# Performance work log

Measured on AMD Instinct MI355X. Metric: run time of the kernel, lower is better.

## Reference

```python
import jax, jax.numpy as jnp
import numpy as np

B, T, D = 1, 2048, 2048
H, HD = 16, 128          # n_heads, head_dim
RD = 64                  # rotary_emb_dim
K = 4                    # short conv kernel size
EPS = 1e-5


def setup_inputs() -> dict:
    key = jax.random.key(0)
    ks = jax.random.split(key, 10)
    hidden_states = jax.random.normal(ks[0], (B, T, D), dtype=jnp.float32)
    # standard RoPE tables for the rotary sub-dimension
    inv_freq = 1.0 / (10000.0 ** (jnp.arange(0, RD, 2, dtype=jnp.float32) / RD))  # [RD/2]
    pos = jnp.arange(T, dtype=jnp.float32)
    freqs = pos[:, None] * inv_freq[None, :]          # [T, RD/2]
    emb = jnp.concatenate([freqs, freqs], axis=-1)    # [T, RD]
    cos = jnp.broadcast_to(jnp.cos(emb)[None], (B, T, RD))
    sin = jnp.broadcast_to(jnp.sin(emb)[None], (B, T, RD))
    s = 1.0 / np.sqrt(D)
    return {
        "hidden_states": hidden_states,
        "cos": cos, "sin": sin,
        "Wq": jax.random.normal(ks[1], (D, D), jnp.float32) * s,
        "Wk": jax.random.normal(ks[2], (D, D), jnp.float32) * s,
        "Wv": jax.random.normal(ks[3], (D, D), jnp.float32) * s,
        "Wo": jax.random.normal(ks[4], (D, D), jnp.float32) * s,
        "conv_q_w": jax.random.normal(ks[5], (D, K), jnp.float32) * 0.5,
        "conv_k_w": jax.random.normal(ks[6], (D, K), jnp.float32) * 0.5,
        "conv_v_w": jax.random.normal(ks[7], (D, K), jnp.float32) * 0.5,
        "q_norm_w": jnp.ones((HD,), jnp.float32),
        "k_norm_w": jnp.ones((HD,), jnp.float32),
    }


def _causal_conv_silu(x, w):
    # x: [B,T,D], w: [D,K]; depthwise causal conv (tap K-1 hits current pos) + SiLU
    xp = jnp.pad(x, ((0, 0), (K - 1, 0), (0, 0)))
    y = sum(xp[:, j:j + T, :] * w[None, None, :, j] for j in range(K))
    return jax.nn.silu(y)


def _rms_norm(x, w):
    # x: [..., HD]
    var = jnp.mean(x * x, axis=-1, keepdims=True)
    return x * jax.lax.rsqrt(var + EPS) * w


def _rotate_half(x):
    x1, x2 = x[..., : x.shape[-1] // 2], x[..., x.shape[-1] // 2:]
    return jnp.concatenate([-x2, x1], axis=-1)


def _apply_rope(x, cos, sin):
    # x: [B,H,T,HD]; cos/sin: [B,T,RD] -> unsqueeze head dim; partial rotary branch
    cos = cos[:, None, :, :]
    sin = sin[:, None, :, :]
    x_rot, x_pass = x[..., :RD], x[..., RD:]
    x_rot = x_rot * cos + _rotate_half(x_rot) * sin
    # faithful to source: negates rotated part when rotary_dim != head_dim
    return jnp.concatenate([-x_rot, x_pass], axis=-1)


def reference(hidden_states, cos, sin, Wq, Wk, Wv, Wo,
              conv_q_w, conv_k_w, conv_v_w, q_norm_w, k_norm_w):
    # projections (Linear with bias=False: y = x @ W^T)
    q = hidden_states @ Wq.T
    k = hidden_states @ Wk.T
    v = hidden_states @ Wv.T
    # short causal depthwise conv + SiLU
    q = _causal_conv_silu(q, conv_q_w)
    k = _causal_conv_silu(k, conv_k_w)
    v = _causal_conv_silu(v, conv_v_w)
    # split heads: [B,T,D] -> [B,T,H,HD]
    q = q.reshape(B, T, H, HD)
    k = k.reshape(B, T, H, HD)
    v = v.reshape(B, T, H, HD)
    # per-head RMSNorm, then [B,H,T,HD]
    q = _rms_norm(q, q_norm_w).transpose(0, 2, 1, 3)
    k = _rms_norm(k, k_norm_w).transpose(0, 2, 1, 3)
    v = v.transpose(0, 2, 1, 3)
    # RoPE (partial)
    q = _apply_rope(q, cos, sin)
    k = _apply_rope(k, cos, sin)
    # causal attention
    scale = 1.0 / np.sqrt(HD)
    scores = jnp.einsum('bhqd,bhkd->bhqk', q, k) * scale
    causal = jnp.tril(jnp.ones((T, T), dtype=bool))
    scores = jnp.where(causal[None, None], scores, jnp.float32(-1e30))
    probs = jax.nn.softmax(scores, axis=-1)
    attn = jnp.einsum('bhqk,bhkd->bhqd', probs, v)
    # [B,H,T,HD] -> [B,T,D], output projection
    out = attn.transpose(0, 2, 1, 3).reshape(B, T, D) @ Wo.T
    return out
```

## Files before the change

kernel.cpp:

```cpp
#include <hip/hip_runtime.h>
#include <hip/hip_bf16.h>

#define T_SEQ 2048
#define D_MODEL 2048
#define NH 16
#define HDIM 128
#define RD_ROT 64

typedef __bf16 bf16x8 __attribute__((ext_vector_type(8)));
typedef float f32x4 __attribute__((ext_vector_type(4)));

__device__ __forceinline__ void async_copy16(const __bf16* g, __bf16* l) {
    __builtin_amdgcn_global_load_lds(
        (const __attribute__((address_space(1))) void*)g,
        (__attribute__((address_space(3))) void*)l, 16, 0, 0);
}

__global__ __launch_bounds__(256) void cast_kernel(
    const float* __restrict__ s0, const float* __restrict__ s1, const float* __restrict__ s2,
    const float* __restrict__ s3, const float* __restrict__ s4,
    __bf16* __restrict__ d0, __bf16* __restrict__ d1, __bf16* __restrict__ d2,
    __bf16* __restrict__ d3, __bf16* __restrict__ d4)
{
    const float* s; __bf16* d;
    switch (blockIdx.y) {
        case 0: s = s0; d = d0; break;
        case 1: s = s1; d = d1; break;
        case 2: s = s2; d = d2; break;
        case 3: s = s3; d = d3; break;
        default: s = s4; d = d4; break;
    }
    size_t base = (size_t)blockIdx.x * D_MODEL + (size_t)threadIdx.x * 8;
    f32x4 a = *(const f32x4*)(s + base);
    f32x4 b = *(const f32x4*)(s + base + 4);
    bf16x8 o;
    #pragma unroll
    for (int i = 0; i < 4; i++) { o[i] = (__bf16)a[i]; o[i + 4] = (__bf16)b[i]; }
    *(bf16x8*)(d + base) = o;
}

__device__ __forceinline__ bf16x8 ld_frag(const __bf16* lds, int rr, int s, int quad, int r7) {
    return *(const bf16x8*)&lds[rr * 64 + ((((s << 2) + quad) ^ r7) << 3)];
}

__global__ __launch_bounds__(512, 2) void gemm_qkv_8ph_kernel(
    const __bf16* __restrict__ A,
    const __bf16* __restrict__ B0, const __bf16* __restrict__ B1, const __bf16* __restrict__ B2,
    __bf16* __restrict__ C0, __bf16* __restrict__ C1, __bf16* __restrict__ C2)
{
    constexpr int BM = 256, BK = 64, KD = D_MODEL, NT = KD / BK;

    __shared__ __align__(16) __bf16 As[2][BM * BK];
    __shared__ __align__(16) __bf16 Bs[2][BM * BK];

    const int flat = (int)blockIdx.x + 8 * ((int)blockIdx.y + 8 * (int)blockIdx.z);
    const int swz  = (flat & 7) * 24 + (flat >> 3);
    const int bz   = swz >> 6;
    const int bm   = (swz & 7) * BM;
    const int bn   = ((swz >> 3) & 7) * BM;

    const __bf16* Bmat = bz == 0 ? B0 : (bz == 1 ? B1 : B2);
    __bf16* Cmat       = bz == 0 ? C0 : (bz == 1 ? C1 : C2);

    const int tid  = threadIdx.x;
    const int lane = tid & 63;
    const int wave = tid >> 6;
    const int r15  = lane & 15;
    const int quad = lane >> 4;
    const int r7   = r15 & 7;
    const int wm   = wave >> 2;
    const int wn   = wave & 3;

    const int sr8 = lane >> 3;
    const int sck = (lane & 7) ^ sr8;
    const __bf16* Ap = A    + (size_t)(bm + wave * 16 + sr8) * KD + sck * 8;
    const __bf16* Bp = Bmat + (size_t)(bn + wave * 16 + sr8) * KD + sck * 8;

    auto stageA = [&](int buf, int h, int kt) {
        const __bf16* s = Ap + (size_t)(h * 128) * KD + kt;
        __bf16* d = &As[buf][h * 8192 + wave * 1024];
        async_copy16(s, d);
        async_copy16(s + 8 * KD, d + 512);
    };
    auto stageB = [&](int buf, int h, int kt) {
        const __bf16* s = Bp + (size_t)(h * 128) * KD + kt;
        __bf16* d = &Bs[buf][h * 8192 + wave * 1024];
        async_copy16(s, d);
        async_copy16(s + 8 * KD, d + 512);
    };

    f32x4 acc[8][4] = {};

    stageA(0, 0, 0);  stageA(0, 1, 0);  stageB(0, 0, 0);  stageB(0, 1, 0);
    stageA(1, 0, BK); stageA(1, 1, BK); stageB(1, 0, BK); stageB(1, 1, BK);
    asm volatile("s_waitcnt vmcnt(8)" ::: "memory");
    __builtin_amdgcn_s_barrier();

    for (int t = 0; t < NT; t++) {
        const int b = t & 1;
        const __bf16* Asb = As[b];
        const __bf16* Bsb = Bs[b];
        const bool pf = (t + 2 < NT);
        const int ktp = (t + 2) * BK;

        bf16x8 a0[4][2], a1[4][2], b0[2][2], b1[2][2];

        #pragma unroll
        for (int mf = 0; mf < 4; mf++)
            #pragma unroll
            for (int s = 0; s < 2; s++)
                a0[mf][s] = ld_frag(Asb, wm * 128 + mf * 16 + r15, s, quad, r7);
        #pragma unroll
        for (int nf = 0; nf < 2; nf++)
            #pragma unroll
            for (int s = 0; s < 2; s++)
                b0[nf][s] = ld_frag(Bsb, wn * 64 + nf * 16 + r15, s, quad, r7);
        __builtin_amdgcn_s_barrier();
        asm volatile("s_waitcnt lgkmcnt(0)" ::: "memory");
        __builtin_amdgcn_sched_barrier(0);
        __builtin_amdgcn_s_setprio(1);
        #pragma unroll
        for (int mf = 0; mf < 4; mf++)
            #pragma unroll
            for (int nf = 0; nf < 2; nf++)
                #pragma unroll
                for (int s = 0; s < 2; s++)
                    acc[mf][nf] = __builtin_amdgcn_mfma_f32_16x16x32_bf16(a0[mf][s], b0[nf][s], acc[mf][nf], 0, 0, 0);
        __builtin_amdgcn_s_setprio(0);
        __builtin_amdgcn_sched_barrier(0);
        __builtin_amdgcn_s_barrier();

        #pragma unroll
        for (int mf = 0; mf < 4; mf++)
            #pragma unroll
            for (int s = 0; s < 2; s++)
                a1[mf][s] = ld_frag(Asb, wm * 128 + 64 + mf * 16 + r15, s, quad, r7);
        #pragma unroll
        for (int nf = 0; nf < 2; nf++)
            #pragma unroll
            for (int s = 0; s < 2; s++)
                b1[nf][s] = ld_frag(Bsb, wn * 64 + 32 + nf * 16 + r15, s, quad, r7);
        __builtin_amdgcn_s_barrier();
        asm volatile("s_waitcnt lgkmcnt(0)" ::: "memory");
        __builtin_amdgcn_sched_barrier(0);
        __builtin_amdgcn_s_setprio(1);
        #pragma unroll
        for (int mf = 0; mf < 4; mf++)
            #pragma unroll
            for (int nf = 0; nf < 2; nf++)
                #pragma unroll
                for (int s = 0; s < 2; s++)
                    acc[4 + mf][2 + nf] = __builtin_amdgcn_mfma_f32_16x16x32_bf16(a1[mf][s], b1[nf][s], acc[4 + mf][2 + nf], 0, 0, 0);
        __builtin_amdgcn_s_setprio(0);
        __builtin_amdgcn_sched_barrier(0);
        __builtin_amdgcn_s_barrier();

        if (pf) { stageA(b, 0, ktp); stageB(b, 0, ktp); }
        __builtin_amdgcn_s_barrier();
        __builtin_amdgcn_s_setprio(1);
        #pragma unroll
        for (int mf = 0; mf < 4; mf++)
            #pragma unroll
            for (int nf = 0; nf < 2; nf++)
                #pragma unroll
                for (int s = 0; s < 2; s++)
                    acc[mf][2 + nf] = __builtin_amdgcn_mfma_f32_16x16x32_bf16(a0[mf][s], b1[nf][s], acc[mf][2 + nf], 0, 0, 0);
        __builtin_amdgcn_s_setprio(0);
        __builtin_amdgcn_sched_barrier(0);
        __builtin_amdgcn_s_barrier();

        if (pf) { stageA(b, 1, ktp); stageB(b, 1, ktp); }
        __builtin_amdgcn_s_barrier();
        __builtin_amdgcn_s_setprio(1);
        #pragma unroll
        for (int mf = 0; mf < 4; mf++)
            #pragma unroll
            for (int nf = 0; nf < 2; nf++)
                #pragma unroll
                for (int s = 0; s < 2; s++)
                    acc[4 + mf][nf] = __builtin_amdgcn_mfma_f32_16x16x32_bf16(a1[mf][s], b0[nf][s], acc[4 + mf][nf], 0, 0, 0);
        __builtin_amdgcn_s_setprio(0);
        __builtin_amdgcn_sched_barrier(0);
        if (t + 1 < NT) {
            if (pf) asm volatile("s_waitcnt vmcnt(8)" ::: "memory");
            else    asm volatile("s_waitcnt vmcnt(0)" ::: "memory");
        }
        __builtin_amdgcn_s_barrier();
    }

    #pragma unroll
    for (int mf = 0; mf < 8; mf++) {
        #pragma unroll
        for (int r = 0; r < 4; r++) {
            const size_t row = (size_t)(bm + wm * 128 + mf * 16 + quad * 4 + r);
            #pragma unroll
            for (int nf = 0; nf < 4; nf++) {
                const size_t col = (size_t)(bn + wn * 64 + nf * 16 + r15);
                Cmat[row * D_MODEL + col] = (__bf16)acc[mf][nf][r];
            }
        }
    }
}

__global__ __launch_bounds__(256) void gemm_bt_splitk_kernel(
    const __bf16* __restrict__ A, const __bf16* __restrict__ Bm, float* __restrict__ C)
{
    constexpr int BM = 128, BK = 32, KD = D_MODEL, NIT = (KD / 2) / BK;
    __shared__ __align__(16) __bf16 As[2][BM * BK];
    __shared__ __align__(16) __bf16 Bs[2][BM * BK];

    const int lane = threadIdx.x & 63;
    const int wave = threadIdx.x >> 6;
    const int r15  = lane & 15;
    const int quad = lane >> 4;
    const int bm = blockIdx.x * BM;
    const int bn = blockIdx.y * BM;
    const int wm = (wave >> 1) * 64;
    const int wn = (wave & 1) * 64;
    const int kbase = blockIdx.z * (KD / 2);

    f32x4 acc[4][4] = {};
    const int srow = wave * 32 + (lane >> 2);
    const int sg   = (lane & 3) ^ ((lane >> 2) & 3);

    const __bf16* Arow0 = A  + (size_t)(bm + srow)      * KD + kbase + sg * 8;
    const __bf16* Arow1 = A  + (size_t)(bm + srow + 16) * KD + kbase + sg * 8;
    const __bf16* Brow0 = Bm + (size_t)(bn + srow)      * KD + kbase + sg * 8;
    const __bf16* Brow1 = Bm + (size_t)(bn + srow + 16) * KD + kbase + sg * 8;

    async_copy16(Arow0, &As[0][wave * 1024]);
    async_copy16(Arow1, &As[0][wave * 1024 + 512]);
    async_copy16(Brow0, &Bs[0][wave * 1024]);
    async_copy16(Brow1, &Bs[0][wave * 1024 + 512]);

    for (int it = 0; it < NIT; it++) {
        const int buf = it & 1;
        __syncthreads();

        if (it + 1 < NIT) {
            const int k0 = (it + 1) * BK;
            const int nb = buf ^ 1;
            async_copy16(Arow0 + k0, &As[nb][wave * 1024]);
            async_copy16(Arow1 + k0, &As[nb][wave * 1024 + 512]);
            async_copy16(Brow0 + k0, &Bs[nb][wave * 1024]);
            async_copy16(Brow1 + k0, &Bs[nb][wave * 1024 + 512]);
        }

        bf16x8 av[4], bv[4];
        #pragma unroll
        for (int mt = 0; mt < 4; mt++)
            av[mt] = *(const bf16x8*)&As[buf][(wm + mt * 16 + r15) * BK + ((quad ^ (r15 & 3)) << 3)];
        #pragma unroll
        for (int nt = 0; nt < 4; nt++)
            bv[nt] = *(const bf16x8*)&Bs[buf][(wn + nt * 16 + r15) * BK + ((quad ^ (r15 & 3)) << 3)];
        #pragma unroll
        for (int mt = 0; mt < 4; mt++)
            #pragma unroll
            for (int nt = 0; nt < 4; nt++)
                acc[mt][nt] = __builtin_amdgcn_mfma_f32_16x16x32_bf16(av[mt], bv[nt], acc[mt][nt], 0, 0, 0);
    }

    #pragma unroll
    for (int mt = 0; mt < 4; mt++) {
        #pragma unroll
        for (int r = 0; r < 4; r++) {
            size_t row = bm + wm + mt * 16 + quad * 4 + r;
            #pragma unroll
            for (int nt = 0; nt < 4; nt++) {
                size_t col = bn + wn + nt * 16 + r15;
                atomicAdd(&C[row * D_MODEL + col], acc[mt][nt][r]);
            }
        }
    }
}

__global__ __launch_bounds__(256) void preproc_qk_kernel(
    const __bf16* __restrict__ q_raw, const __bf16* __restrict__ k_raw,
    const float* __restrict__ cwq, const float* __restrict__ cwk,
    const float* __restrict__ qnw, const float* __restrict__ knw,
    const float* __restrict__ cosb, const float* __restrict__ sinb,
    __bf16* __restrict__ q_proc, __bf16* __restrict__ k_proc)
{
    const int t = blockIdx.x;
    const int which = blockIdx.y;
    const __bf16* X = which ? k_raw : q_raw;
    const float*  W = which ? cwk : cwq;
    const float*  nw = which ? knw : qnw;
    __bf16* P = which ? k_proc : q_proc;
    const float SC = which ? 1.0f : 0.08838834764831845f;

    const int tid = threadIdx.x;
    const int c0  = tid * 8;
    const int h   = tid >> 4;
    const int dl0 = (tid & 15) * 8;

    f32x4 wv[8];
    #pragma unroll
    for (int i = 0; i < 8; i++) wv[i] = *(const f32x4*)&W[(c0 + i) * 4];

    float acc[8] = {};
    #pragma unroll
    for (int j = 0; j < 4; j++) {
        int tt = t + j - 3;
        if (tt >= 0) {
            bf16x8 xv = *(const bf16x8*)&X[(size_t)tt * D_MODEL + c0];
            #pragma unroll
            for (int i = 0; i < 8; i++) acc[i] += (float)xv[i] * wv[i][j];
        }
    }
    float sil[8], ss = 0.f;
    #pragma unroll
    for (int i = 0; i < 8; i++) {
        float s = acc[i] / (1.f + __expf(-acc[i]));
        sil[i] = s; ss += s * s;
    }
    #pragma unroll
    for (int off = 1; off < 16; off <<= 1) ss += __shfl_xor(ss, off);
    float inv = rsqrtf(ss * (1.f / 128.f) + 1e-5f);

    f32x4 nv0 = *(const f32x4*)&nw[dl0];
    f32x4 nv1 = *(const f32x4*)&nw[dl0 + 4];
    float yn[8];
    #pragma unroll
    for (int i = 0; i < 8; i++) yn[i] = sil[i] * inv * (i < 4 ? nv0[i] : nv1[i - 4]);

    float partner[8];
    #pragma unroll
    for (int i = 0; i < 8; i++) partner[i] = __shfl_xor(yn[i], 4);

    bf16x8 o;
    if (dl0 < RD_ROT) {
        f32x4 cv0 = *(const f32x4*)&cosb[t * RD_ROT + dl0];
        f32x4 cv1 = *(const f32x4*)&cosb[t * RD_ROT + dl0 + 4];
        f32x4 sv0 = *(const f32x4*)&sinb[t * RD_ROT + dl0];
        f32x4 sv1 = *(const f32x4*)&sinb[t * RD_ROT + dl0 + 4];
        #pragma unroll
        for (int i = 0; i < 8; i++) {
            int dl = dl0 + i;
            float c = i < 4 ? cv0[i] : cv1[i - 4];
            float s = i < 4 ? sv0[i] : sv1[i - 4];
            float rot = (dl < 32) ? -partner[i] : partner[i];
            o[i] = (__bf16)((yn[i] * c + rot * s) * SC);
        }
    } else {
        #pragma unroll
        for (int i = 0; i < 8; i++) o[i] = (__bf16)(yn[i] * SC);
    }
    *(bf16x8*)&P[((size_t)h * T_SEQ + t) * HDIM + dl0] = o;
}

__global__ __launch_bounds__(128) void preproc_v_kernel(
    const __bf16* __restrict__ v_raw, const float* __restrict__ cwv,
    __bf16* __restrict__ v_t)
{
    const int t0 = blockIdx.x * 8;
    const int h = blockIdx.y;
    const int dl = threadIdx.x;
    const int d = h * HDIM + dl;

    f32x4 wv = *(const f32x4*)&cwv[d * 4];
    float x[11];
    #pragma unroll
    for (int m = 0; m < 11; m++) {
        int tt = t0 - 3 + m;
        x[m] = (tt >= 0) ? (float)v_raw[(size_t)tt * D_MODEL + d] : 0.f;
    }
    bf16x8 o;
    #pragma unroll
    for (int r = 0; r < 8; r++) {
        float y = x[r] * wv[0] + x[r + 1] * wv[1] + x[r + 2] * wv[2] + x[r + 3] * wv[3];
        o[r] = (__bf16)(y / (1.f + __expf(-y)));
    }
    *(bf16x8*)&v_t[((size_t)h * HDIM + dl) * T_SEQ + t0] = o;
}

__global__ __launch_bounds__(256, 2) void attn_kernel(
    const __bf16* __restrict__ Qp,
    const __bf16* __restrict__ Kp,
    const __bf16* __restrict__ Vt,
    __bf16* __restrict__ Op)
{
    constexpr int TK = 64, PSTR = 72;
    __shared__ __align__(16) __bf16 Ks[2][TK * HDIM];
    __shared__ __align__(16) __bf16 Vs[2][HDIM * TK];
    __shared__ __align__(16) __bf16 Ps[64 * PSTR];

    const int lane = threadIdx.x & 63;
    const int wave = threadIdx.x >> 6;
    const int r15  = lane & 15;
    const int quad = lane >> 4;
    const int h = blockIdx.y;
    const int qi = (blockIdx.y & 8) ? ((int)gridDim.x - 1 - (int)blockIdx.x) : (int)blockIdx.x;
    const int q0 = qi * TK;

    const __bf16* Kb = Kp + (size_t)h * T_SEQ * HDIM;
    const __bf16* Vb = Vt + (size_t)h * HDIM * T_SEQ;

    const int kchunk = wave * 4;
    const int krow_l = (lane >> 4);
    const int kg     = lane & 15;
    const int vrow_l = (lane >> 3);
    const int vg     = lane & 7;

    bf16x8 qf[4];
    const __bf16* qbase = Qp + ((size_t)h * T_SEQ + q0 + wave * 16 + r15) * HDIM;
    #pragma unroll
    for (int s = 0; s < 4; s++) qf[s] = *(const bf16x8*)(qbase + s * 32 + quad * 8);

    f32x4 oacc[8] = {};
    float lsum[4] = {};

    const int ntk = qi + 1;

    #pragma unroll
    for (int i = 0; i < 4; i++) {
        int ck = kchunk + i;
        int krow = ck * 4 + krow_l;
        int vrow = ck * 8 + vrow_l;
        async_copy16(Kb + (size_t)krow * HDIM + (kg ^ (krow & 15)) * 8, &Ks[0][ck * 512]);
        async_copy16(Vb + (size_t)vrow * T_SEQ + (vg ^ (vrow & 7)) * 8, &Vs[0][ck * 512]);
    }

    for (int it = 0; it < ntk; it++) {
        const int buf = it & 1;
        const bool last = (it == ntk - 1);
        __syncthreads();

        if (!last) {
            const int tkn = (it + 1) * TK;
            const int nbuf = buf ^ 1;
            #pragma unroll
            for (int i = 0; i < 4; i++) {
                int ck = kchunk + i;
                int krow = ck * 4 + krow_l;
                int vrow = ck * 8 + vrow_l;
                async_copy16(Kb + (size_t)(tkn + krow) * HDIM + (kg ^ (krow & 15)) * 8, &Ks[nbuf][ck * 512]);
                async_copy16(Vb + (size_t)vrow * T_SEQ + tkn + (vg ^ (vrow & 7)) * 8, &Vs[nbuf][ck * 512]);
            }
        }

        f32x4 sacc[4] = {};
        #pragma unroll
        for (int s = 0; s < 4; s++) {
            #pragma unroll
            for (int nt = 0; nt < 4; nt++) {
                bf16x8 kf = *(const bf16x8*)&Ks[buf][(nt * 16 + r15) * HDIM + (((s * 4 + quad) ^ r15) << 3)];
                sacc[nt] = __builtin_amdgcn_mfma_f32_16x16x32_bf16(qf[s], kf, sacc[nt], 0, 0, 0);
            }
        }

        #pragma unroll
        for (int nt = 0; nt < 4; nt++) {
            #pragma unroll
            for (int r = 0; r < 4; r++) {
                float p = __expf(sacc[nt][r]);
                if (last) {
                    int qrow = q0 + wave * 16 + quad * 4 + r;
                    int kcol = it * TK + nt * 16 + r15;
                    if (kcol > qrow) p = 0.f;
                }
                sacc[nt][r] = p;
                lsum[r] += p;
            }
        }

        #pragma unroll
        for (int nt = 0; nt < 4; nt++)
            #pragma unroll
            for (int r = 0; r < 4; r++)
                Ps[(wave * 16 + quad * 4 + r) * PSTR + nt * 16 + r15] = (__bf16)sacc[nt][r];

        #pragma unroll
        for (int s2 = 0; s2 < 2; s2++) {
            bf16x8 pf = *(const bf16x8*)&Ps[(wave * 16 + r15) * PSTR + s2 * 32 + quad * 8];
            #pragma unroll
            for (int nt = 0; nt < 8; nt++) {
                bf16x8 vf = *(const bf16x8*)&Vs[buf][(nt * 16 + r15) * TK + (((s2 * 4 + quad) ^ (r15 & 7)) << 3)];
                oacc[nt] = __builtin_amdgcn_mfma_f32_16x16x32_bf16(pf, vf, oacc[nt], 0, 0, 0);
            }
        }
    }

    #pragma unroll
    for (int r = 0; r < 4; r++) {
        float l = lsum[r];
        #pragma unroll
        for (int off = 1; off < 16; off <<= 1) l += __shfl_xor(l, off);
        float inv = 1.0f / l;
        size_t row = q0 + wave * 16 + quad * 4 + r;
        #pragma unroll
        for (int nt = 0; nt < 8; nt++)
            Op[row * D_MODEL + h * HDIM + nt * 16 + r15] = (__bf16)(oacc[nt][r] * inv);
    }
}

extern "C" void kernel_launch(void* const* d_in, const int* in_sizes, int n_in,
                              void* d_out, int out_size, void* d_ws, size_t ws_size,
                              hipStream_t stream) {
    (void)in_sizes; (void)n_in; (void)out_size; (void)ws_size;
    const float* hidden = (const float*)d_in[0];
    const float* cosb   = (const float*)d_in[1];
    const float* sinb   = (const float*)d_in[2];
    const float* Wq     = (const float*)d_in[3];
    const float* Wk     = (const float*)d_in[4];
    const float* Wv     = (const float*)d_in[5];
    const float* Wo     = (const float*)d_in[6];
    const float* cwq    = (const float*)d_in[7];
    const float* cwk    = (const float*)d_in[8];
    const float* cwv    = (const float*)d_in[9];
    const float* qnw    = (const float*)d_in[10];
    const float* knw    = (const float*)d_in[11];

    const size_t NEL = (size_t)T_SEQ * D_MODEL;
    __bf16* ws = (__bf16*)d_ws;
    __bf16* h_bf   = ws + 0 * NEL;
    __bf16* Wq_bf  = ws + 1 * NEL;
    __bf16* Wk_bf  = ws + 2 * NEL;
    __bf16* Wv_bf  = ws + 3 * NEL;
    __bf16* Wo_bf  = ws + 4 * NEL;
    __bf16* q_raw  = ws + 5 * NEL;
    __bf16* k_raw  = ws + 6 * NEL;
    __bf16* v_raw  = ws + 7 * NEL;
    __bf16* q_proc = Wq_bf;
    __bf16* k_proc = Wk_bf;
    __bf16* v_t    = Wv_bf;
    __bf16* attn_b = h_bf;
    float*  out    = (float*)d_out;

    cast_kernel<<<dim3(T_SEQ, 5), 256, 0, stream>>>(hidden, Wq, Wk, Wv, Wo,
                                                    h_bf, Wq_bf, Wk_bf, Wv_bf, Wo_bf);
    gemm_qkv_8ph_kernel<<<dim3(8, 8, 3), 512, 0, stream>>>(
        h_bf, Wq_bf, Wk_bf, Wv_bf, q_raw, k_raw, v_raw);
    preproc_qk_kernel<<<dim3(T_SEQ, 2), 256, 0, stream>>>(
        q_raw, k_raw, cwq, cwk, qnw, knw, cosb, sinb, q_proc, k_proc);
    preproc_v_kernel<<<dim3(T_SEQ / 8, NH), 128, 0, stream>>>(v_raw, cwv, v_t);
    attn_kernel<<<dim3(T_SEQ / 64, NH), 256, 0, stream>>>(q_proc, k_proc, v_t, attn_b);
    hipMemsetAsync(d_out, 0, NEL * sizeof(float), stream);
    gemm_bt_splitk_kernel<<<dim3(16, 16, 2), 256, 0, stream>>>(attn_b, Wo_bf, out);
}
```

Before: 340.8 us.

## Software-pipeline LDS fragment loads across iterations in QKV GEMM

Restructures the QKV GEMM main loop so that LDS fragment reads for the next phase, and for the next k-tile's a0/b0, are issued before or during the current MFMA block. This removes the explicit lgkmcnt(0) waits and halves the number of barriers per iteration. Global prefetch of B and A tiles is split across phases with a vmcnt(4) wait. It adds register pressure because fragments stay live across iterations, and its correctness depends on subtle ordering between the buffer reuse and the barriers.

```diff
diff --git a/kernel.cpp b/kernel.cpp
--- a/kernel.cpp
+++ b/kernel.cpp
@@ -43,7 +43,7 @@
     return *(const bf16x8*)&lds[rr * 64 + ((((s << 2) + quad) ^ r7) << 3)];
 }
 
-__global__ __launch_bounds__(512, 2) void gemm_qkv_8ph_kernel(
+__global__ __launch_bounds__(512, 2) void gemm_qkv_pipe_kernel(
     const __bf16* __restrict__ A,
     const __bf16* __restrict__ B0, const __bf16* __restrict__ B1, const __bf16* __restrict__ B2,
     __bf16* __restrict__ C0, __bf16* __restrict__ C1, __bf16* __restrict__ C2)
@@ -90,102 +90,100 @@
     };
 
     f32x4 acc[8][4] = {};
-
-    stageA(0, 0, 0);  stageA(0, 1, 0);  stageB(0, 0, 0);  stageB(0, 1, 0);
-    stageA(1, 0, BK); stageA(1, 1, BK); stageB(1, 0, BK); stageB(1, 1, BK);
+    bf16x8 a0[4][2], a1[4][2], b0[2][2], b1[2][2];
+
+    auto mfma16 = [&](int mb, int nb, bf16x8 (&av)[4][2], bf16x8 (&bv)[2][2]) {
+        #pragma unroll
+        for (int mf = 0; mf < 4; mf++)
+            #pragma unroll
+            for (int nf = 0; nf < 2; nf++)
+                #pragma unroll
+                for (int s = 0; s < 2; s++)
+                    acc[mb + mf][nb + nf] =
+                        __builtin_amdgcn_mfma_f32_16x16x32_bf16(av[mf][s], bv[nf][s], acc[mb + mf][nb + nf], 0, 0, 0);
+    };
+
+    stageB(0, 0, 0);  stageB(0, 1, 0);  stageA(0, 0, 0);  stageA(0, 1, 0);
+    stageB(1, 0, BK); stageB(1, 1, BK); stageA(1, 0, BK); stageA(1, 1, BK);
     asm volatile("s_waitcnt vmcnt(8)" ::: "memory");
     __builtin_amdgcn_s_barrier();
+    __builtin_amdgcn_sched_barrier(0);
+    #pragma unroll
+    for (int mf = 0; mf < 4; mf++)
+        #pragma unroll
+        for (int s = 0; s < 2; s++)
+            a0[mf][s] = ld_frag(As[0], wm * 128 + mf * 16 + r15, s, quad, r7);
+    #pragma unroll
+    for (int nf = 0; nf < 2; nf++)
+        #pragma unroll
+        for (int s = 0; s < 2; s++)
+            b0[nf][s] = ld_frag(Bs[0], wn * 64 + nf * 16 + r15, s, quad, r7);
 
     for (int t = 0; t < NT; t++) {
         const int b = t & 1;
         const __bf16* Asb = As[b];
         const __bf16* Bsb = Bs[b];
+        const __bf16* Aso = As[b ^ 1];
+        const __bf16* Bso = Bs[b ^ 1];
         const bool pf = (t + 2 < NT);
         const int ktp = (t + 2) * BK;
 
-        bf16x8 a0[4][2], a1[4][2], b0[2][2], b1[2][2];
-
-        #pragma unroll
-        for (int mf = 0; mf < 4; mf++)
+        #pragma unroll
+        for (int nf = 0; nf < 2; nf++)
             #pragma unroll
             for (int s = 0; s < 2; s++)
-                a0[mf][s] = ld_frag(Asb, wm * 128 + mf * 16 + r15, s, quad, r7);
-        #pragma unroll
-        for (int nf = 0; nf < 2; nf++)
-            #pragma unroll
-            for (int s = 0; s < 2; s++)
-                b0[nf][s] = ld_frag(Bsb, wn * 64 + nf * 16 + r15, s, quad, r7);
+                b1[nf][s] = ld_frag(Bsb, wn * 64 + 32 + nf * 16 + r15, s, quad, r7);
+        __builtin_amdgcn_sched_barrier(0);
+        __builtin_amdgcn_s_setprio(1);
+        mfma16(0, 0, a0, b0);
+        __builtin_amdgcn_s_setprio(0);
+        __builtin_amdgcn_sched_barrier(0);
         __builtin_amdgcn_s_barrier();
-        asm volatile("s_waitcnt lgkmcnt(0)" ::: "memory");
-        __builtin_amdgcn_sched_barrier(0);
-        __builtin_amdgcn_s_setprio(1);
-        #pragma unroll
-        for (int mf = 0; mf < 4; mf++)
-            #pragma unroll
-            for (int nf = 0; nf < 2; nf++)
-                #pragma unroll
-                for (int s = 0; s < 2; s++)
-                    acc[mf][nf] = __builtin_amdgcn_mfma_f32_16x16x32_bf16(a0[mf][s], b0[nf][s], acc[mf][nf], 0, 0, 0);
-        __builtin_amdgcn_s_setprio(0);
-        __builtin_amdgcn_sched_barrier(0);
-        __builtin_amdgcn_s_barrier();
+        __builtin_amdgcn_sched_barrier(0);
 
         #pragma unroll
         for (int mf = 0; mf < 4; mf++)
             #pragma unroll
             for (int s = 0; s < 2; s++)
                 a1[mf][s] = ld_frag(Asb, wm * 128 + 64 + mf * 16 + r15, s, quad, r7);
+        __builtin_amdgcn_sched_barrier(0);
+        __builtin_amdgcn_s_setprio(1);
+        mfma16(0, 2, a0, b1);
+        __builtin_amdgcn_s_setprio(0);
+        __builtin_amdgcn_sched_barrier(0);
+        __builtin_amdgcn_s_barrier();
+        __builtin_amdgcn_sched_barrier(0);
+
+        if (pf) { stageB(b, 0, ktp); stageB(b, 1, ktp); }
+        __builtin_amdgcn_sched_barrier(0);
+        __builtin_amdgcn_s_setprio(1);
+        mfma16(4, 2, a1, b1);
+        __builtin_amdgcn_s_setprio(0);
+        __builtin_amdgcn_sched_barrier(0);
+        if (pf) asm volatile("s_waitcnt vmcnt(4)" ::: "memory");
+        else    asm volatile("s_waitcnt vmcnt(0)" ::: "memory");
+        __builtin_amdgcn_s_barrier();
+        __builtin_amdgcn_sched_barrier(0);
+
+        #pragma unroll
+        for (int mf = 0; mf < 4; mf++)
+            #pragma unroll
+            for (int s = 0; s < 2; s++)
+                a0[mf][s] = ld_frag(Aso, wm * 128 + mf * 16 + r15, s, quad, r7);
+        if (pf) { stageA(b, 0, ktp); stageA(b, 1, ktp); }
+        __builtin_amdgcn_sched_barrier(0);
+        __builtin_amdgcn_s_setprio(1);
+        mfma16(4, 0, a1, b0);
+        __builtin_amdgcn_s_setprio(0);
+        __builtin_amdgcn_sched_barrier(0);
         #pragma unroll
         for (int nf = 0; nf < 2; nf++)
             #pragma unroll
             for (int s = 0; s < 2; s++)
-                b1[nf][s] = ld_frag(Bsb, wn * 64 + 32 + nf * 16 + r15, s, quad, r7);
+                b0[nf][s] = ld_frag(Bso, wn * 64 + nf * 16 + r15, s, quad, r7);
+        __builtin_amdgcn_sched_barrier(0);
         __builtin_amdgcn_s_barrier();
-        asm volatile("s_waitcnt lgkmcnt(0)" ::: "memory");
-        __builtin_amdgcn_sched_barrier(0);
-        __builtin_amdgcn_s_setprio(1);
-        #pragma unroll
-        for (int mf = 0; mf < 4; mf++)
-            #pragma unroll
-            for (int nf = 0; nf < 2; nf++)
-                #pragma unroll
-                for (int s = 0; s < 2; s++)
-                    acc[4 + mf][2 + nf] = __builtin_amdgcn_mfma_f32_16x16x32_bf16(a1[mf][s], b1[nf][s], acc[4 + mf][2 + nf], 0, 0, 0);
-        __builtin_amdgcn_s_setprio(0);
-        __builtin_amdgcn_sched_barrier(0);
-        __builtin_amdgcn_s_barrier();
-
-        if (pf) { stageA(b, 0, ktp); stageB(b, 0, ktp); }
-        __builtin_amdgcn_s_barrier();
-        __builtin_amdgcn_s_setprio(1);
-        #pragma unroll
-        for (int mf = 0; mf < 4; mf++)
-            #pragma unroll
-            for (int nf = 0; nf < 2; nf++)
-                #pragma unroll
-                for (int s = 0; s < 2; s++)
-                    acc[mf][2 + nf] = __builtin_amdgcn_mfma_f32_16x16x32_bf16(a0[mf][s], b1[nf][s], acc[mf][2 + nf], 0, 0, 0);
-        __builtin_amdgcn_s_setprio(0);
-        __builtin_amdgcn_sched_barrier(0);
-        __builtin_amdgcn_s_barrier();
-
-        if (pf) { stageA(b, 1, ktp); stageB(b, 1, ktp); }
-        __builtin_amdgcn_s_barrier();
-        __builtin_amdgcn_s_setprio(1);
-        #pragma unroll
-        for (int mf = 0; mf < 4; mf++)
-            #pragma unroll
-            for (int nf = 0; nf < 2; nf++)
-                #pragma unroll
-                for (int s = 0; s < 2; s++)
-                    acc[4 + mf][nf] = __builtin_amdgcn_mfma_f32_16x16x32_bf16(a1[mf][s], b0[nf][s], acc[4 + mf][nf], 0, 0, 0);
-        __builtin_amdgcn_s_setprio(0);
-        __builtin_amdgcn_sched_barrier(0);
-        if (t + 1 < NT) {
-            if (pf) asm volatile("s_waitcnt vmcnt(8)" ::: "memory");
-            else    asm volatile("s_waitcnt vmcnt(0)" ::: "memory");
-        }
-        __builtin_amdgcn_s_barrier();
+        __builtin_amdgcn_sched_barrier(0);
     }
 
     #pragma unroll
@@ -529,7 +527,7 @@
 
     cast_kernel<<<dim3(T_SEQ, 5), 256, 0, stream>>>(hidden, Wq, Wk, Wv, Wo,
                                                     h_bf, Wq_bf, Wk_bf, Wv_bf, Wo_bf);
-    gemm_qkv_8ph_kernel<<<dim3(8, 8, 3), 512, 0, stream>>>(
+    gemm_qkv_pipe_kernel<<<dim3(8, 8, 3), 512, 0, stream>>>(
         h_bf, Wq_bf, Wk_bf, Wv_bf, q_raw, k_raw, v_raw);
     preproc_qk_kernel<<<dim3(T_SEQ, 2), 256, 0, stream>>>(
         q_raw, k_raw, cwq, cwk, qnw, knw, cosb, sinb, q_proc, k_proc);
```

New measurement: 333.2 us. -2.2%, faster.
